# Optimization experiments

Hardware: AMD Instinct MI355X
Metric: run time of the kernel (lower is better)

## Reference

```python
import jax, jax.numpy as jnp
import numpy as np

T, H, E, I, K = 2048, 2048, 16, 512, 2
ROUTED_SCALE = 1.5   # config.moe_router_scaling_factor
SWIGLU_LIMIT = 7.0   # config.swiglu_limits[layer_id]


def setup_inputs() -> dict:
    key = jax.random.key(0)
    k1, k2, k3, k4, k5 = jax.random.split(key, 5)
    hidden_states = jax.random.normal(k1, (T, H), jnp.float32)
    gate_w = jax.random.normal(k2, (E, H), jnp.float32) * 0.02
    router_bias = jax.random.normal(k3, (E,), jnp.float32) * 0.01
    w13 = jax.random.normal(k4, (E, 2 * I, H), jnp.float32) * 0.02  # [gate; up] fused
    w2 = jax.random.normal(k5, (E, H, I), jnp.float32) * 0.02
    return {"hidden_states": hidden_states, "gate_w": gate_w,
            "router_bias": router_bias, "w13": w13, "w2": w2, "top_k": K}


def reference(hidden_states, gate_w, router_bias, w13, w2, top_k):
    n_tok = hidden_states.shape[0]
    n_exp = gate_w.shape[0]
    # fp32 gate (need_fp32_gate=True)
    router_logits = hidden_states.astype(jnp.float32) @ gate_w.T          # [T, E]
    scores = jax.nn.sigmoid(router_logits)
    # correction bias only affects expert choice, not the combine weights
    _, topk_ids = jax.lax.top_k(scores + router_bias[None, :], top_k)     # [T, K]
    topk_w = jnp.take_along_axis(scores, topk_ids, axis=1)                # [T, K]
    topk_w = topk_w / jnp.sum(topk_w, axis=1, keepdims=True)              # renormalize
    topk_w = topk_w * ROUTED_SCALE
    # scatter routing weights into dense per-expert combine weights [T, E]
    comb = jnp.zeros((n_tok, n_exp), jnp.float32)
    comb = comb.at[jnp.arange(n_tok)[:, None], topk_ids].add(topk_w)
    # expert SwiGLU MLPs, dense over experts (zero combine weight == not routed)
    gu = jnp.einsum('th,eoh->teo', hidden_states, w13)                    # [T, E, 2I]
    g, u = jnp.split(gu, 2, axis=-1)
    g = jnp.minimum(g, SWIGLU_LIMIT)                                      # gemm1_clamp_limit
    u = jnp.clip(u, -SWIGLU_LIMIT, SWIGLU_LIMIT)
    act = g * jax.nn.sigmoid(g) * u                                       # silu(gate) * up
    expert_out = jnp.einsum('tei,ehi->teh', act, w2)                      # [T, E, H]
    return jnp.einsum('teh,te->th', expert_out, comb)                     # [T, H]
```

## Files before the change

### kernel.cpp

```cpp
#include <hip/hip_runtime.h>
#include <hip/hip_bf16.h>
#include <math.h>

#define T_TOK 2048
#define H_DIM 2048
#define E_EXP 16
#define I_DIM 512
#define TWO_I 1024
#define ROUTED_SCALE 1.5f
#define SWIGLU_LIMIT 7.0f

#define BM 128
#define KC 32
#define KC2 64
#define MAX_TILES 48
#define SLOTS 6144

typedef __attribute__((ext_vector_type(8))) short bf16x8;
typedef __attribute__((ext_vector_type(4))) float f32x4;
typedef unsigned short u16;

__device__ inline u16 f2bf(float f) {
    return __builtin_bit_cast(u16, __float2bfloat16(f));
}
__device__ inline ushort4 pack4(float4 a) {
    ushort4 v;
    v.x = f2bf(a.x); v.y = f2bf(a.y); v.z = f2bf(a.z); v.w = f2bf(a.w);
    return v;
}
__device__ inline bf16x8 cvt8(float4 a, float4 b) {
    bf16x8 v;
    v[0] = (short)f2bf(a.x); v[1] = (short)f2bf(a.y);
    v[2] = (short)f2bf(a.z); v[3] = (short)f2bf(a.w);
    v[4] = (short)f2bf(b.x); v[5] = (short)f2bf(b.y);
    v[6] = (short)f2bf(b.z); v[7] = (short)f2bf(b.w);
    return v;
}

__device__ inline void gload16(const u16* g, u16* l) {
    __builtin_amdgcn_global_load_lds(
        (const __attribute__((address_space(1))) void*)(g),
        (__attribute__((address_space(3))) void*)(l), 16, 0, 0);
}
#define SCHED0() __builtin_amdgcn_sched_barrier(0)

#define SWZ(row, k) ((row) * 64 + ((k) ^ (((row) & 7) << 3)))

__global__ __launch_bounds__(256) void router_kernel(
    const float* __restrict__ hs, const float* __restrict__ gw,
    const float* __restrict__ bias, int* cnt, int* tok_list, float* w_list,
    u16* __restrict__ hs_bf)
{
    int w = threadIdx.x >> 6;
    int lane = threadIdx.x & 63;
    int t = blockIdx.x * 2 + (w >> 1);
    int kh = w & 1;
    const float* x = hs + (size_t)t * H_DIM + kh * 1024;
    const float* gwb = gw + kh * 1024;
    u16* hb = hs_bf + (size_t)t * H_DIM + kh * 1024;

    float acc[E_EXP];
#pragma unroll
    for (int e = 0; e < E_EXP; ++e) acc[e] = 0.f;

#pragma unroll
    for (int c = 0; c < 4; ++c) {
        int col = c * 256 + lane * 4;
        float4 xv = *(const float4*)(x + col);
        *(ushort4*)(hb + col) = pack4(xv);
#pragma unroll
        for (int e = 0; e < E_EXP; ++e) {
            float4 gv = *(const float4*)(gwb + (size_t)e * H_DIM + col);
            acc[e] = fmaf(xv.x, gv.x, acc[e]);
            acc[e] = fmaf(xv.y, gv.y, acc[e]);
            acc[e] = fmaf(xv.z, gv.z, acc[e]);
            acc[e] = fmaf(xv.w, gv.w, acc[e]);
        }
    }
#pragma unroll
    for (int e = 0; e < E_EXP; ++e) {
        for (int m = 32; m >= 1; m >>= 1)
            acc[e] += __shfl_xor(acc[e], m, 64);
    }
    __shared__ float part[4][E_EXP];
    if (lane == 0) {
#pragma unroll
        for (int e = 0; e < E_EXP; ++e) part[w][e] = acc[e];
    }
    __syncthreads();
    if (kh == 0 && lane == 0) {
        float sc[E_EXP], bsc[E_EXP];
#pragma unroll
        for (int e = 0; e < E_EXP; ++e) {
            float s = part[w][e] + part[w + 1][e];
            sc[e] = 1.f / (1.f + expf(-s));
            bsc[e] = sc[e] + bias[e];
        }
        int e0 = 0; float b0 = bsc[0];
#pragma unroll
        for (int e = 1; e < E_EXP; ++e) if (bsc[e] > b0) { b0 = bsc[e]; e0 = e; }
        int e1 = -1; float b1 = -1e30f;
#pragma unroll
        for (int e = 0; e < E_EXP; ++e) {
            if (e == e0) continue;
            if (bsc[e] > b1) { b1 = bsc[e]; e1 = e; }
        }
        float s0 = sc[e0], s1 = sc[e1];
        float inv = ROUTED_SCALE / (s0 + s1);
        int p0 = atomicAdd(&cnt[e0], 1);
        tok_list[e0 * T_TOK + p0] = t;
        w_list[e0 * T_TOK + p0] = s0 * inv;
        int p1 = atomicAdd(&cnt[e1], 1);
        tok_list[e1 * T_TOK + p1] = t;
        w_list[e1 * T_TOK + p1] = s1 * inv;
    }
}

__global__ void scatter_build(const int* __restrict__ cnt,
    const int* __restrict__ tok_list, const float* __restrict__ w_list,
    int* A_tok, float* A_w, int* tile_e, int* tile_r0, int* n_slots)
{
    int c[E_EXP], offs[E_EXP + 1];
    offs[0] = 0;
#pragma unroll
    for (int e = 0; e < E_EXP; ++e) {
        c[e] = cnt[e];
        offs[e + 1] = offs[e] + ((c[e] + BM - 1) & ~(BM - 1));
    }
    int idx = blockIdx.x * 256 + threadIdx.x;
    int e = idx >> 11;
    int pos = idx & (T_TOK - 1);
    int ce = c[e];
    int pe = (ce + BM - 1) & ~(BM - 1);
    if (pos < ce) {
        A_tok[offs[e] + pos] = tok_list[idx];
        A_w[offs[e] + pos] = w_list[idx];
    } else if (pos < pe) {
        A_tok[offs[e] + pos] = -1;
        A_w[offs[e] + pos] = 0.f;
    }
    if (idx == 0) {
        int nt = 0;
        for (int ee = 0; ee < E_EXP; ++ee) {
            int ntile = (c[ee] + BM - 1) >> 7;
            for (int j = 0; j < ntile; ++j) {
                tile_e[nt] = ee;
                tile_r0[nt] = offs[ee] + j * BM;
                ++nt;
            }
        }
        for (; nt < MAX_TILES; ++nt) tile_e[nt] = -1;
        *n_slots = offs[E_EXP];
    }
}

__global__ __launch_bounds__(256, 3) void gemm1_gu(
    const u16* __restrict__ hs_bf, const float* __restrict__ w13,
    const int* __restrict__ A_tok, const int* __restrict__ tile_e,
    const int* __restrict__ tile_r0, float* __restrict__ gu_part)
{
    int b = blockIdx.x;
    int y = b & 7;
    int kspl = (b >> 3) & 1;
    int tile = b >> 4;
    int e = tile_e[tile];
    if (e < 0) return;
    int row0 = tile_r0[tile];
    int i0 = y * 64;
    int k0base = kspl * (H_DIM / 2);
    int tid = threadIdx.x;

    __shared__ u16 Xs[2][4096];
    __shared__ u16 Gs[2][2048];
    __shared__ u16 Us[2][2048];

    const int l = tid & 63, w = tid >> 6;

    const u16* sX[2]; int dX[2];
#pragma unroll
    for (int j = 0; j < 2; ++j) {
        int row = w * 32 + j * 16 + (l >> 2);
        int tk = A_tok[row0 + row]; if (tk < 0) tk = 0;
        int sg = (l & 3) ^ ((l >> 3) & 3);
        sX[j] = hs_bf + (size_t)tk * H_DIM + k0base + sg * 8;
        dX[j] = (w * 32 + j * 16) * 32;
    }
#define X_STAGE(bb, t) do { int ko = (t) * KC; \
    gload16(sX[0] + ko, &Xs[bb][dX[0]]); gload16(sX[1] + ko, &Xs[bb][dX[1]]); } while (0)

    const int wr = tid >> 2;
    const int wg = tid & 3;
    const int wsk = (wg ^ ((wr >> 1) & 3)) * 8;
    const float* gsrc = w13 + ((size_t)e * TWO_I + i0 + wr) * H_DIM + k0base + wsk;
    const float* usrc = gsrc + (size_t)I_DIM * H_DIM;
    const int wdst = wr * 32 + wg * 8;

    float4 gA, gB, uA, uB;
#define W_LOAD(t) do { int ko = (t) * KC; \
    gA = *(const float4*)(gsrc + ko); gB = *(const float4*)(gsrc + ko + 4); \
    uA = *(const float4*)(usrc + ko); uB = *(const float4*)(usrc + ko + 4); } while (0)
#define W_WRITE(bb) do { \
    *(bf16x8*)&Gs[bb][wdst] = cvt8(gA, gB); \
    *(bf16x8*)&Us[bb][wdst] = cvt8(uA, uB); } while (0)

    const int wm = w >> 1, wn = w & 1;
    const int lr = l & 15, lg = l >> 4;
    const int swz = (lg ^ ((lr >> 1) & 3)) * 8;
    int ix[4], ib[2];
#pragma unroll
    for (int m = 0; m < 4; ++m) ix[m] = (wm * 64 + m * 16 + lr) * 32 + swz;
#pragma unroll
    for (int n = 0; n < 2; ++n) ib[n] = (wn * 32 + n * 16 + lr) * 32 + swz;

    const f32x4 Z4 = {0.f, 0.f, 0.f, 0.f};
    f32x4 aG[4][2], aU[4][2];
#pragma unroll
    for (int m = 0; m < 4; ++m)
#pragma unroll
        for (int n = 0; n < 2; ++n) { aG[m][n] = Z4; aU[m][n] = Z4; }

    W_LOAD(0);
    X_STAGE(0, 0);
    W_WRITE(0);
    __syncthreads();
    int cur = 0;
    const int NT = (H_DIM / 2) / KC;
    for (int t = 0; t < NT; ++t) {
        const bool more = (t + 1 < NT);
        if (more) {
            X_STAGE(cur ^ 1, t + 1);
            W_LOAD(t + 1);
            SCHED0();
        }
        {
            bf16x8 a0 = *(const bf16x8*)&Xs[cur][ix[0]];
            bf16x8 a1 = *(const bf16x8*)&Xs[cur][ix[1]];
            bf16x8 a2 = *(const bf16x8*)&Xs[cur][ix[2]];
            bf16x8 a3 = *(const bf16x8*)&Xs[cur][ix[3]];
            bf16x8 g0 = *(const bf16x8*)&Gs[cur][ib[0]];
            bf16x8 g1 = *(const bf16x8*)&Gs[cur][ib[1]];
            bf16x8 u0 = *(const bf16x8*)&Us[cur][ib[0]];
            bf16x8 u1 = *(const bf16x8*)&Us[cur][ib[1]];
            aG[0][0] = __builtin_amdgcn_mfma_f32_16x16x32_bf16(a0, g0, aG[0][0], 0, 0, 0);
            aG[0][1] = __builtin_amdgcn_mfma_f32_16x16x32_bf16(a0, g1, aG[0][1], 0, 0, 0);
            aG[1][0] = __builtin_amdgcn_mfma_f32_16x16x32_bf16(a1, g0, aG[1][0], 0, 0, 0);
            aG[1][1] = __builtin_amdgcn_mfma_f32_16x16x32_bf16(a1, g1, aG[1][1], 0, 0, 0);
            aG[2][0] = __builtin_amdgcn_mfma_f32_16x16x32_bf16(a2, g0, aG[2][0], 0, 0, 0);
            aG[2][1] = __builtin_amdgcn_mfma_f32_16x16x32_bf16(a2, g1, aG[2][1], 0, 0, 0);
            aG[3][0] = __builtin_amdgcn_mfma_f32_16x16x32_bf16(a3, g0, aG[3][0], 0, 0, 0);
            aG[3][1] = __builtin_amdgcn_mfma_f32_16x16x32_bf16(a3, g1, aG[3][1], 0, 0, 0);
            aU[0][0] = __builtin_amdgcn_mfma_f32_16x16x32_bf16(a0, u0, aU[0][0], 0, 0, 0);
            aU[0][1] = __builtin_amdgcn_mfma_f32_16x16x32_bf16(a0, u1, aU[0][1], 0, 0, 0);
            aU[1][0] = __builtin_amdgcn_mfma_f32_16x16x32_bf16(a1, u0, aU[1][0], 0, 0, 0);
            aU[1][1] = __builtin_amdgcn_mfma_f32_16x16x32_bf16(a1, u1, aU[1][1], 0, 0, 0);
            aU[2][0] = __builtin_amdgcn_mfma_f32_16x16x32_bf16(a2, u0, aU[2][0], 0, 0, 0);
            aU[2][1] = __builtin_amdgcn_mfma_f32_16x16x32_bf16(a2, u1, aU[2][1], 0, 0, 0);
            aU[3][0] = __builtin_amdgcn_mfma_f32_16x16x32_bf16(a3, u0, aU[3][0], 0, 0, 0);
            aU[3][1] = __builtin_amdgcn_mfma_f32_16x16x32_bf16(a3, u1, aU[3][1], 0, 0, 0);
        }
        if (more) W_WRITE(cur ^ 1);
        __syncthreads();
        cur ^= 1;
    }
#undef X_STAGE
#undef W_LOAD
#undef W_WRITE

    float* gp = gu_part + (size_t)kspl * SLOTS * TWO_I;
#pragma unroll
    for (int m = 0; m < 4; ++m)
#pragma unroll
        for (int n = 0; n < 2; ++n) {
            int col = i0 + wn * 32 + n * 16 + lr;
            int sbase = row0 + wm * 64 + m * 16 + lg * 4;
#pragma unroll
            for (int q = 0; q < 4; ++q) {
                gp[(size_t)(sbase + q) * TWO_I + col]         = aG[m][n][q];
                gp[(size_t)(sbase + q) * TWO_I + I_DIM + col] = aU[m][n][q];
            }
        }
}

__global__ __launch_bounds__(256) void swiglu_pass(
    const float* __restrict__ gu_part, const int* __restrict__ n_slots,
    u16* __restrict__ act)
{
    int idx = blockIdx.x * 256 + threadIdx.x;
    int slot = idx >> 7;
    if (slot >= *n_slots) return;
    int i4 = (idx & 127) << 2;
    const float* p0 = gu_part + (size_t)slot * TWO_I + i4;
    const float* p1 = p0 + (size_t)SLOTS * TWO_I;
    float4 g0 = *(const float4*)p0;
    float4 g1 = *(const float4*)p1;
    float4 u0 = *(const float4*)(p0 + I_DIM);
    float4 u1 = *(const float4*)(p1 + I_DIM);
    float4 r;
    {
        float g = fminf(g0.x + g1.x, SWIGLU_LIMIT);
        float u = fminf(fmaxf(u0.x + u1.x, -SWIGLU_LIMIT), SWIGLU_LIMIT);
        r.x = g * (1.f / (1.f + __expf(-g))) * u;
    }
    {
        float g = fminf(g0.y + g1.y, SWIGLU_LIMIT);
        float u = fminf(fmaxf(u0.y + u1.y, -SWIGLU_LIMIT), SWIGLU_LIMIT);
        r.y = g * (1.f / (1.f + __expf(-g))) * u;
    }
    {
        float g = fminf(g0.z + g1.z, SWIGLU_LIMIT);
        float u = fminf(fmaxf(u0.z + u1.z, -SWIGLU_LIMIT), SWIGLU_LIMIT);
        r.z = g * (1.f / (1.f + __expf(-g))) * u;
    }
    {
        float g = fminf(g0.w + g1.w, SWIGLU_LIMIT);
        float u = fminf(fmaxf(u0.w + u1.w, -SWIGLU_LIMIT), SWIGLU_LIMIT);
        r.w = g * (1.f / (1.f + __expf(-g))) * u;
    }
    *(ushort4*)(act + (size_t)slot * I_DIM + i4) = pack4(r);
}

__global__ __launch_bounds__(256, 3) void gemm2_scatter(
    const u16* __restrict__ act, const float* __restrict__ w2,
    const int* __restrict__ A_tok, const float* __restrict__ A_w,
    const int* __restrict__ tile_e, const int* __restrict__ tile_r0,
    float* __restrict__ out)
{
    int b = blockIdx.x;
    int id = (b & 7) * 192 + (b >> 3);
    int tile = id % MAX_TILES;
    int y = id / MAX_TILES;
    int e = tile_e[tile];
    if (e < 0) return;
    int row0 = tile_r0[tile];
    int h0 = y * 64;
    int tid = threadIdx.x;

    __shared__ u16 As[2][8192];
    __shared__ u16 Bs[2][4096];

    const int l = tid & 63, w = tid >> 6;

    const int rlo = l >> 3;
    const int c8 = (l & 7) << 3;
    const int ksrc = c8 ^ (rlo << 3);
    const u16* sA[4];
#pragma unroll
    for (int j = 0; j < 4; ++j) {
        int row = w * 32 + j * 8 + rlo;
        sA[j] = act + (size_t)(row0 + row) * I_DIM + ksrc;
    }
    const int dA = w * 2048;

#define A_STAGE(bb, t) do { int ko = (t) * KC2; \
    gload16(sA[0] + ko, &As[bb][dA]); \
    gload16(sA[1] + ko, &As[bb][dA + 512]); \
    gload16(sA[2] + ko, &As[bb][dA + 1024]); \
    gload16(sA[3] + ko, &As[bb][dA + 1536]); } while (0)

    const int srow = tid >> 4;
    const int sc4  = tid & 15;
    const int kphys = (sc4 * 4) ^ ((srow & 7) << 3);
    const int sbase = srow * 64 + kphys;
    const float* bsrc = w2 + ((size_t)e * H_DIM + h0 + srow) * I_DIM + sc4 * 4;

    float4 bld[4];
#define B_LOAD(t) do { int k0 = (t) * KC2; \
    bld[0] = *(const float4*)(bsrc + k0); \
    bld[1] = *(const float4*)(bsrc + k0 + 16 * I_DIM); \
    bld[2] = *(const float4*)(bsrc + k0 + 32 * I_DIM); \
    bld[3] = *(const float4*)(bsrc + k0 + 48 * I_DIM); } while (0)

#define B_WRITE(bb) do { \
    *(ushort4*)&Bs[bb][sbase]        = pack4(bld[0]); \
    *(ushort4*)&Bs[bb][sbase + 1024] = pack4(bld[1]); \
    *(ushort4*)&Bs[bb][sbase + 2048] = pack4(bld[2]); \
    *(ushort4*)&Bs[bb][sbase + 3072] = pack4(bld[3]); } while (0)

    const int wm = w >> 1, wn = w & 1;
    const int lr = l & 15, lg = l >> 4;
    int ia[4][2], ib2[2][2];
#pragma unroll
    for (int kh = 0; kh < 2; ++kh) {
        int e2 = kh * 32 + lg * 8;
#pragma unroll
        for (int m = 0; m < 4; ++m) ia[m][kh] = SWZ(wm * 64 + m * 16 + lr, e2);
#pragma unroll
        for (int n = 0; n < 2; ++n) ib2[n][kh] = SWZ(wn * 32 + n * 16 + lr, e2);
    }

    const f32x4 Z4 = {0.f, 0.f, 0.f, 0.f};
    f32x4 acc[4][2];
#pragma unroll
    for (int m = 0; m < 4; ++m)
#pragma unroll
        for (int n = 0; n < 2; ++n) acc[m][n] = Z4;

    B_LOAD(0);
    A_STAGE(0, 0);
    B_WRITE(0);
    __syncthreads();
    int cur = 0;
    const int NT = I_DIM / KC2;
    for (int t = 0; t < NT; ++t) {
        const bool more = (t + 1 < NT);
        if (more) {
            A_STAGE(cur ^ 1, t + 1);
            B_LOAD(t + 1);
            SCHED0();
        }
#pragma unroll
        for (int kh = 0; kh < 2; ++kh) {
            bf16x8 a0 = *(const bf16x8*)&As[cur][ia[0][kh]];
            bf16x8 a1 = *(const bf16x8*)&As[cur][ia[1][kh]];
            bf16x8 a2 = *(const bf16x8*)&As[cur][ia[2][kh]];
            bf16x8 a3 = *(const bf16x8*)&As[cur][ia[3][kh]];
            bf16x8 b0 = *(const bf16x8*)&Bs[cur][ib2[0][kh]];
            bf16x8 b1 = *(const bf16x8*)&Bs[cur][ib2[1][kh]];
            acc[0][0] = __builtin_amdgcn_mfma_f32_16x16x32_bf16(a0, b0, acc[0][0], 0, 0, 0);
            acc[0][1] = __builtin_amdgcn_mfma_f32_16x16x32_bf16(a0, b1, acc[0][1], 0, 0, 0);
            acc[1][0] = __builtin_amdgcn_mfma_f32_16x16x32_bf16(a1, b0, acc[1][0], 0, 0, 0);
            acc[1][1] = __builtin_amdgcn_mfma_f32_16x16x32_bf16(a1, b1, acc[1][1], 0, 0, 0);
            acc[2][0] = __builtin_amdgcn_mfma_f32_16x16x32_bf16(a2, b0, acc[2][0], 0, 0, 0);
            acc[2][1] = __builtin_amdgcn_mfma_f32_16x16x32_bf16(a2, b1, acc[2][1], 0, 0, 0);
            acc[3][0] = __builtin_amdgcn_mfma_f32_16x16x32_bf16(a3, b0, acc[3][0], 0, 0, 0);
            acc[3][1] = __builtin_amdgcn_mfma_f32_16x16x32_bf16(a3, b1, acc[3][1], 0, 0, 0);
        }
        if (more) B_WRITE(cur ^ 1);
        __syncthreads();
        cur ^= 1;
    }
#undef A_STAGE
#undef B_LOAD
#undef B_WRITE

#pragma unroll
    for (int m = 0; m < 4; ++m)
#pragma unroll
        for (int n = 0; n < 2; ++n) {
            int col = h0 + wn * 32 + n * 16 + lr;
            int sb = row0 + wm * 64 + m * 16 + lg * 4;
#pragma unroll
            for (int q = 0; q < 4; ++q) {
                int slot = sb + q;
                int tok = A_tok[slot];
                if (tok >= 0)
                    atomicAdd(&out[(size_t)tok * H_DIM + col], acc[m][n][q] * A_w[slot]);
            }
        }
}

extern "C" void kernel_launch(void* const* d_in, const int* in_sizes, int n_in,
                              void* d_out, int out_size, void* d_ws, size_t ws_size,
                              hipStream_t stream) {
    const float* hs   = (const float*)d_in[0];
    const float* gw   = (const float*)d_in[1];
    const float* bias = (const float*)d_in[2];
    const float* w13  = (const float*)d_in[3];
    const float* w2   = (const float*)d_in[4];
    float* out = (float*)d_out;

    char* ws = (char*)d_ws;
    int*   cnt      = (int*)(ws + 0);
    int*   n_slots  = (int*)(ws + 64);
    int*   tile_e   = (int*)(ws + 128);
    int*   tile_r0  = (int*)(ws + 384);
    int*   tok_list = (int*)(ws + 1024);
    float* w_list   = (float*)(ws + 132096);
    int*   A_tok    = (int*)(ws + 263168);
    float* A_w      = (float*)(ws + 287744);
    u16*   act      = (u16*)(ws + 315392);
    u16*   hs_bf    = (u16*)(ws + 6606848);
    float* gu_part  = (float*)(ws + 14995456);

    hipMemsetAsync(d_out, 0, (size_t)T_TOK * H_DIM * sizeof(float), stream);
    hipMemsetAsync(cnt, 0, 64, stream);

    router_kernel<<<T_TOK / 2, 256, 0, stream>>>(hs, gw, bias, cnt, tok_list, w_list, hs_bf);
    scatter_build<<<(E_EXP * T_TOK) / 256, 256, 0, stream>>>(cnt, tok_list, w_list, A_tok, A_w, tile_e, tile_r0, n_slots);

    gemm1_gu<<<MAX_TILES * 8 * 2, 256, 0, stream>>>(hs_bf, w13, A_tok, tile_e, tile_r0, gu_part);
    swiglu_pass<<<SLOTS * I_DIM / 4 / 256, 256, 0, stream>>>(gu_part, n_slots, act);
    gemm2_scatter<<<MAX_TILES * 32, 256, 0, stream>>>(act, w2, A_tok, A_w, tile_e, tile_r0, out);
}
```

Baseline: 205.0 us.

## Add XCD-aware job lists, 4-way K split, bf16 partials, smaller gemm2 tiles

Builds per-XCD job queues in scatter_build so that blocks working on the same expert's weights land on the same XCD (blockIdx & 7) and only valid tiles get launched. Gemm1 now splits K four ways instead of two and writes its partial sums as bf16 instead of fp32, and swiglu sums the four partials. Gemm2 drops to 64-row tiles with higher occupancy, which gives more parallel jobs but also more W2 loads and atomics. The bf16 partials lose some accuracy, and the extra K split adds partial-buffer traffic.

```diff
diff --git a/kernel.cpp b/kernel.cpp
--- a/kernel.cpp
+++ b/kernel.cpp
@@ -15,6 +15,8 @@
 #define KC2 64
 #define MAX_TILES 48
 #define SLOTS 6144
+#define NSPL 4
+#define JCAP 512
 
 typedef __attribute__((ext_vector_type(8))) short bf16x8;
 typedef __attribute__((ext_vector_type(4))) float f32x4;
@@ -22,6 +24,10 @@
 
 __device__ inline u16 f2bf(float f) {
     return __builtin_bit_cast(u16, __float2bfloat16(f));
+}
+__device__ inline float bf2f(u16 h) {
+    unsigned int u = ((unsigned int)h) << 16;
+    return __builtin_bit_cast(float, u);
 }
 __device__ inline ushort4 pack4(float4 a) {
     ushort4 v;
@@ -118,7 +124,8 @@
 
 __global__ void scatter_build(const int* __restrict__ cnt,
     const int* __restrict__ tok_list, const float* __restrict__ w_list,
-    int* A_tok, float* A_w, int* tile_e, int* tile_r0, int* n_slots)
+    int* A_tok, float* A_w, int* tile_e, int* tile_r0, int* n_slots,
+    int* jobs1, int* jobs2)
 {
     int c[E_EXP], offs[E_EXP + 1];
     offs[0] = 0;
@@ -141,11 +148,27 @@
     }
     if (idx == 0) {
         int nt = 0;
+        int c1[8], c2[8];
+#pragma unroll
+        for (int x = 0; x < 8; ++x) { c1[x] = 0; c2[x] = 0; }
         for (int ee = 0; ee < E_EXP; ++ee) {
             int ntile = (c[ee] + BM - 1) >> 7;
             for (int j = 0; j < ntile; ++j) {
-                tile_e[nt] = ee;
-                tile_r0[nt] = offs[ee] + j * BM;
+                int t = nt;
+                tile_e[t] = ee;
+                tile_r0[t] = offs[ee] + j * BM;
+                for (int kspl = 0; kspl < NSPL; ++kspl) {
+                    int x = (ee * 4 + kspl) & 7;
+                    for (int y = 0; y < 8; ++y)
+                        jobs1[x * JCAP + c1[x]++] = t * 32 + y * 4 + kspl;
+                }
+                for (int s = 0; s < 2; ++s) {
+                    int t2 = t * 2 + s;
+                    for (int y = 0; y < 32; ++y) {
+                        int x = (ee + y) & 7;
+                        jobs2[x * JCAP + c2[x]++] = t2 * 32 + y;
+                    }
+                }
                 ++nt;
             }
         }
@@ -157,17 +180,19 @@
 __global__ __launch_bounds__(256, 3) void gemm1_gu(
     const u16* __restrict__ hs_bf, const float* __restrict__ w13,
     const int* __restrict__ A_tok, const int* __restrict__ tile_e,
-    const int* __restrict__ tile_r0, float* __restrict__ gu_part)
+    const int* __restrict__ tile_r0, const int* __restrict__ jobs1,
+    u16* __restrict__ gu_part)
 {
     int b = blockIdx.x;
-    int y = b & 7;
-    int kspl = (b >> 3) & 1;
-    int tile = b >> 4;
+    int job = jobs1[(b & 7) * JCAP + (b >> 3)];
+    if (job < 0) return;
+    int kspl = job & 3;
+    int y = (job >> 2) & 7;
+    int tile = job >> 5;
     int e = tile_e[tile];
-    if (e < 0) return;
     int row0 = tile_r0[tile];
     int i0 = y * 64;
-    int k0base = kspl * (H_DIM / 2);
+    int k0base = kspl * (H_DIM / NSPL);
     int tid = threadIdx.x;
 
     __shared__ u16 Xs[2][4096];
@@ -224,7 +249,7 @@
     W_WRITE(0);
     __syncthreads();
     int cur = 0;
-    const int NT = (H_DIM / 2) / KC;
+    const int NT = (H_DIM / NSPL) / KC;
     for (int t = 0; t < NT; ++t) {
         const bool more = (t + 1 < NT);
         if (more) {
@@ -266,7 +291,7 @@
 #undef W_LOAD
 #undef W_WRITE
 
-    float* gp = gu_part + (size_t)kspl * SLOTS * TWO_I;
+    u16* gp = gu_part + (size_t)kspl * SLOTS * TWO_I;
 #pragma unroll
     for (int m = 0; m < 4; ++m)
 #pragma unroll
@@ -275,67 +300,58 @@
             int sbase = row0 + wm * 64 + m * 16 + lg * 4;
 #pragma unroll
             for (int q = 0; q < 4; ++q) {
-                gp[(size_t)(sbase + q) * TWO_I + col]         = aG[m][n][q];
-                gp[(size_t)(sbase + q) * TWO_I + I_DIM + col] = aU[m][n][q];
+                gp[(size_t)(sbase + q) * TWO_I + col]         = f2bf(aG[m][n][q]);
+                gp[(size_t)(sbase + q) * TWO_I + I_DIM + col] = f2bf(aU[m][n][q]);
             }
         }
 }
 
 __global__ __launch_bounds__(256) void swiglu_pass(
-    const float* __restrict__ gu_part, const int* __restrict__ n_slots,
+    const u16* __restrict__ gu_part, const int* __restrict__ n_slots,
     u16* __restrict__ act)
 {
     int idx = blockIdx.x * 256 + threadIdx.x;
     int slot = idx >> 7;
     if (slot >= *n_slots) return;
     int i4 = (idx & 127) << 2;
-    const float* p0 = gu_part + (size_t)slot * TWO_I + i4;
-    const float* p1 = p0 + (size_t)SLOTS * TWO_I;
-    float4 g0 = *(const float4*)p0;
-    float4 g1 = *(const float4*)p1;
-    float4 u0 = *(const float4*)(p0 + I_DIM);
-    float4 u1 = *(const float4*)(p1 + I_DIM);
+    const u16* base = gu_part + (size_t)slot * TWO_I + i4;
+    float g[4] = {0.f, 0.f, 0.f, 0.f}, u[4] = {0.f, 0.f, 0.f, 0.f};
+#pragma unroll
+    for (int k = 0; k < NSPL; ++k) {
+        const u16* p = base + (size_t)k * SLOTS * TWO_I;
+        ushort4 gv = *(const ushort4*)p;
+        ushort4 uv = *(const ushort4*)(p + I_DIM);
+        g[0] += bf2f(gv.x); g[1] += bf2f(gv.y); g[2] += bf2f(gv.z); g[3] += bf2f(gv.w);
+        u[0] += bf2f(uv.x); u[1] += bf2f(uv.y); u[2] += bf2f(uv.z); u[3] += bf2f(uv.w);
+    }
     float4 r;
-    {
-        float g = fminf(g0.x + g1.x, SWIGLU_LIMIT);
-        float u = fminf(fmaxf(u0.x + u1.x, -SWIGLU_LIMIT), SWIGLU_LIMIT);
-        r.x = g * (1.f / (1.f + __expf(-g))) * u;
-    }
-    {
-        float g = fminf(g0.y + g1.y, SWIGLU_LIMIT);
-        float u = fminf(fmaxf(u0.y + u1.y, -SWIGLU_LIMIT), SWIGLU_LIMIT);
-        r.y = g * (1.f / (1.f + __expf(-g))) * u;
-    }
-    {
-        float g = fminf(g0.z + g1.z, SWIGLU_LIMIT);
-        float u = fminf(fmaxf(u0.z + u1.z, -SWIGLU_LIMIT), SWIGLU_LIMIT);
-        r.z = g * (1.f / (1.f + __expf(-g))) * u;
-    }
-    {
-        float g = fminf(g0.w + g1.w, SWIGLU_LIMIT);
-        float u = fminf(fmaxf(u0.w + u1.w, -SWIGLU_LIMIT), SWIGLU_LIMIT);
-        r.w = g * (1.f / (1.f + __expf(-g))) * u;
+    float* rp = &r.x;
+#pragma unroll
+    for (int j = 0; j < 4; ++j) {
+        float gg = fminf(g[j], SWIGLU_LIMIT);
+        float uu = fminf(fmaxf(u[j], -SWIGLU_LIMIT), SWIGLU_LIMIT);
+        rp[j] = gg * (1.f / (1.f + __expf(-gg))) * uu;
     }
     *(ushort4*)(act + (size_t)slot * I_DIM + i4) = pack4(r);
 }
 
-__global__ __launch_bounds__(256, 3) void gemm2_scatter(
+__global__ __launch_bounds__(256, 4) void gemm2_scatter(
     const u16* __restrict__ act, const float* __restrict__ w2,
     const int* __restrict__ A_tok, const float* __restrict__ A_w,
     const int* __restrict__ tile_e, const int* __restrict__ tile_r0,
-    float* __restrict__ out)
+    const int* __restrict__ jobs2, float* __restrict__ out)
 {
     int b = blockIdx.x;
-    int id = (b & 7) * 192 + (b >> 3);
-    int tile = id % MAX_TILES;
-    int y = id / MAX_TILES;
-    int e = tile_e[tile];
-    if (e < 0) return;
-    int row0 = tile_r0[tile];
+    int job = jobs2[(b & 7) * JCAP + (b >> 3)];
+    if (job < 0) return;
+    int y = job & 31;
+    int tile2 = job >> 5;
+    int e = tile_e[tile2 >> 1];
+    int row0 = tile_r0[tile2 >> 1] + (tile2 & 1) * 64;
     int h0 = y * 64;
     int tid = threadIdx.x;
 
-    __shared__ u16 As[2][8192];
+    __shared__ u16 As[2][4096];
     __shared__ u16 Bs[2][4096];
 
     const int l = tid & 63, w = tid >> 6;
@@ -343,19 +359,14 @@
     const int rlo = l >> 3;
     const int c8 = (l & 7) << 3;
     const int ksrc = c8 ^ (rlo << 3);
-    const u16* sA[4];
-#pragma unroll
-    for (int j = 0; j < 4; ++j) {
-        int row = w * 32 + j * 8 + rlo;
-        sA[j] = act + (size_t)(row0 + row) * I_DIM + ksrc;
-    }
-    const int dA = w * 2048;
+    const int rowA = w * 16 + rlo;
+    const int rowB = rowA + 8;
+    const u16* sAA = act + (size_t)(row0 + rowA) * I_DIM + ksrc;
+    const u16* sAB = act + (size_t)(row0 + rowB) * I_DIM + ksrc;
+    const int dA = w * 1024;
 
 #define A_STAGE(bb, t) do { int ko = (t) * KC2; \
-    gload16(sA[0] + ko, &As[bb][dA]); \
-    gload16(sA[1] + ko, &As[bb][dA + 512]); \
-    gload16(sA[2] + ko, &As[bb][dA + 1024]); \
-    gload16(sA[3] + ko, &As[bb][dA + 1536]); } while (0)
+    gload16(sAA + ko, &As[bb][dA]);  gload16(sAB + ko, &As[bb][dA + 512]); } while (0)
 
     const int srow = tid >> 4;
     const int sc4  = tid & 15;
@@ -377,21 +388,22 @@
     *(ushort4*)&Bs[bb][sbase + 3072] = pack4(bld[3]); } while (0)
 
     const int wm = w >> 1, wn = w & 1;
-    const int lr = l & 15, lg = l >> 4;
-    int ia[4][2], ib2[2][2];
+    const int lr = l & 15;
+    const int lg = l >> 4;
+    const int ra0 = wm * 32 + lr, ra1 = ra0 + 16;
+    const int rb0 = wn * 32 + lr, rb1 = rb0 + 16;
+    int ia0[2], ia1[2], ib0[2], ib1[2];
 #pragma unroll
     for (int kh = 0; kh < 2; ++kh) {
         int e2 = kh * 32 + lg * 8;
-#pragma unroll
-        for (int m = 0; m < 4; ++m) ia[m][kh] = SWZ(wm * 64 + m * 16 + lr, e2);
-#pragma unroll
-        for (int n = 0; n < 2; ++n) ib2[n][kh] = SWZ(wn * 32 + n * 16 + lr, e2);
+        ia0[kh] = SWZ(ra0, e2); ia1[kh] = SWZ(ra1, e2);
+        ib0[kh] = SWZ(rb0, e2); ib1[kh] = SWZ(rb1, e2);
     }
 
     const f32x4 Z4 = {0.f, 0.f, 0.f, 0.f};
-    f32x4 acc[4][2];
-#pragma unroll
-    for (int m = 0; m < 4; ++m)
+    f32x4 acc[2][2];
+#pragma unroll
+    for (int m = 0; m < 2; ++m)
 #pragma unroll
         for (int n = 0; n < 2; ++n) acc[m][n] = Z4;
 
@@ -410,20 +422,14 @@
         }
 #pragma unroll
         for (int kh = 0; kh < 2; ++kh) {
-            bf16x8 a0 = *(const bf16x8*)&As[cur][ia[0][kh]];
-            bf16x8 a1 = *(const bf16x8*)&As[cur][ia[1][kh]];
-            bf16x8 a2 = *(const bf16x8*)&As[cur][ia[2][kh]];
-            bf16x8 a3 = *(const bf16x8*)&As[cur][ia[3][kh]];
-            bf16x8 b0 = *(const bf16x8*)&Bs[cur][ib2[0][kh]];
-            bf16x8 b1 = *(const bf16x8*)&Bs[cur][ib2[1][kh]];
+            bf16x8 a0 = *(const bf16x8*)&As[cur][ia0[kh]];
+            bf16x8 a1 = *(const bf16x8*)&As[cur][ia1[kh]];
+            bf16x8 b0 = *(const bf16x8*)&Bs[cur][ib0[kh]];
+            bf16x8 b1 = *(const bf16x8*)&Bs[cur][ib1[kh]];
             acc[0][0] = __builtin_amdgcn_mfma_f32_16x16x32_bf16(a0, b0, acc[0][0], 0, 0, 0);
             acc[0][1] = __builtin_amdgcn_mfma_f32_16x16x32_bf16(a0, b1, acc[0][1], 0, 0, 0);
             acc[1][0] = __builtin_amdgcn_mfma_f32_16x16x32_bf16(a1, b0, acc[1][0], 0, 0, 0);
             acc[1][1] = __builtin_amdgcn_mfma_f32_16x16x32_bf16(a1, b1, acc[1][1], 0, 0, 0);
-            acc[2][0] = __builtin_amdgcn_mfma_f32_16x16x32_bf16(a2, b0, acc[2][0], 0, 0, 0);
-            acc[2][1] = __builtin_amdgcn_mfma_f32_16x16x32_bf16(a2, b1, acc[2][1], 0, 0, 0);
-            acc[3][0] = __builtin_amdgcn_mfma_f32_16x16x32_bf16(a3, b0, acc[3][0], 0, 0, 0);
-            acc[3][1] = __builtin_amdgcn_mfma_f32_16x16x32_bf16(a3, b1, acc[3][1], 0, 0, 0);
         }
         if (more) B_WRITE(cur ^ 1);
         __syncthreads();
@@ -434,14 +440,14 @@
 #undef B_WRITE
 
 #pragma unroll
-    for (int m = 0; m < 4; ++m)
+    for (int m = 0; m < 2; ++m)
 #pragma unroll
         for (int n = 0; n < 2; ++n) {
             int col = h0 + wn * 32 + n * 16 + lr;
-            int sb = row0 + wm * 64 + m * 16 + lg * 4;
+            int sb = wm * 32 + m * 16 + lg * 4;
 #pragma unroll
             for (int q = 0; q < 4; ++q) {
-                int slot = sb + q;
+                int slot = row0 + sb + q;
                 int tok = A_tok[slot];
                 if (tok >= 0)
                     atomicAdd(&out[(size_t)tok * H_DIM + col], acc[m][n][q] * A_w[slot]);
@@ -464,21 +470,25 @@
     int*   n_slots  = (int*)(ws + 64);
     int*   tile_e   = (int*)(ws + 128);
     int*   tile_r0  = (int*)(ws + 384);
-    int*   tok_list = (int*)(ws + 1024);
-    float* w_list   = (float*)(ws + 132096);
-    int*   A_tok    = (int*)(ws + 263168);
-    float* A_w      = (float*)(ws + 287744);
-    u16*   act      = (u16*)(ws + 315392);
-    u16*   hs_bf    = (u16*)(ws + 6606848);
-    float* gu_part  = (float*)(ws + 14995456);
+    int*   jobs1    = (int*)(ws + 1024);
+    int*   jobs2    = (int*)(ws + 17408);
+    int*   tok_list = (int*)(ws + 33792);
+    float* w_list   = (float*)(ws + 164864);
+    int*   A_tok    = (int*)(ws + 295936);
+    float* A_w      = (float*)(ws + 320512);
+    u16*   act      = (u16*)(ws + 345088);
+    u16*   hs_bf    = (u16*)(ws + 6636544);
+    u16*   gu_part  = (u16*)(ws + 15025152);
 
     hipMemsetAsync(d_out, 0, (size_t)T_TOK * H_DIM * sizeof(float), stream);
     hipMemsetAsync(cnt, 0, 64, stream);
+    hipMemsetAsync(jobs1, 0xFF, 2 * 8 * JCAP * sizeof(int), stream);
 
     router_kernel<<<T_TOK / 2, 256, 0, stream>>>(hs, gw, bias, cnt, tok_list, w_list, hs_bf);
-    scatter_build<<<(E_EXP * T_TOK) / 256, 256, 0, stream>>>(cnt, tok_list, w_list, A_tok, A_w, tile_e, tile_r0, n_slots);
-
-    gemm1_gu<<<MAX_TILES * 8 * 2, 256, 0, stream>>>(hs_bf, w13, A_tok, tile_e, tile_r0, gu_part);
+    scatter_build<<<(E_EXP * T_TOK) / 256, 256, 0, stream>>>(cnt, tok_list, w_list,
+        A_tok, A_w, tile_e, tile_r0, n_slots, jobs1, jobs2);
+
+    gemm1_gu<<<8 * JCAP, 256, 0, stream>>>(hs_bf, w13, A_tok, tile_e, tile_r0, jobs1, gu_part);
     swiglu_pass<<<SLOTS * I_DIM / 4 / 256, 256, 0, stream>>>(gu_part, n_slots, act);
-    gemm2_scatter<<<MAX_TILES * 32, 256, 0, stream>>>(act, w2, A_tok, A_w, tile_e, tile_r0, out);
-}
+    gemm2_scatter<<<8 * JCAP, 256, 0, stream>>>(act, w2, A_tok, A_w, tile_e, tile_r0, jobs2, out);
+}
```

Result: slower. 434.5 us (+111.9%).
